# Kernel tuning notes

Measured on AMD Instinct MI355X. Metric: run time of the kernel, lower is better.

## Reference

```python
import jax, jax.numpy as jnp
import numpy as np

C = 1.0          # ball curvature (Manifold default)
EPS = 1e-7
MIN_NORM = 1e-15

def _artanh(x):
    return jnp.arctanh(jnp.clip(x, -1.0 + EPS, 1.0 - EPS))

def _expmap0(u):
    # exp map at origin of the Poincare ball
    n = jnp.clip(jnp.linalg.norm(u, axis=-1, keepdims=True), MIN_NORM, None)
    sc = np.sqrt(C).astype(np.float32)
    return jnp.tanh(sc * n) * u / (sc * n)

def _mobius_add(x, y):
    x2 = jnp.sum(x * x, axis=-1, keepdims=True)
    y2 = jnp.sum(y * y, axis=-1, keepdims=True)
    xy = jnp.sum(x * y, axis=-1, keepdims=True)
    num = (1.0 + 2.0 * C * xy + C * y2) * x + (1.0 - C * x2) * y
    den = 1.0 + 2.0 * C * xy + C * C * x2 * y2
    return num / jnp.clip(den, MIN_NORM, None)

def setup_inputs() -> dict:
    key = jax.random.key(0)
    k1, k2, k3, k4 = jax.random.split(key, 4)
    N, D, U = 8192, 256, 128
    features = jax.random.normal(k1, (N, D), jnp.float32) * 0.1
    adj = jax.random.randint(k2, (N, N), 0, 2, jnp.int32)
    kernel = jax.random.normal(k3, (D, U), jnp.float32) * (1.0 / np.sqrt(D)).astype(np.float32)
    bias = jax.random.normal(k4, (U,), jnp.float32) * 0.01
    return {"features": features, "adj": adj, "kernel": kernel, "bias": bias}

def reference(features, adj, kernel, bias):
    sc = np.sqrt(C).astype(np.float32)
    # dense matmul then lift to the ball
    x = _expmap0(features @ kernel)                     # [N, U]
    # pairwise hyperbolic distance via closed form of ||mobius_add(-x_i, x_j)||
    x2 = jnp.sum(x * x, axis=-1)                        # [N]
    xy = x @ x.T                                        # [N, N]
    A = 1.0 - 2.0 * C * xy + C * x2[None, :]            # [N, N]
    B = (1.0 - C * x2)[:, None]                         # [N, 1]
    num_sq = A * A * x2[:, None] - 2.0 * A * B * xy + B * B * x2[None, :]
    den = 1.0 - 2.0 * C * xy + C * C * x2[:, None] * x2[None, :]
    mnorm = jnp.sqrt(jnp.clip(num_sq, 0.0, None)) / jnp.clip(den, MIN_NORM, None)
    dist = (2.0 / sc) * _artanh(sc * mnorm)             # sqdist ** 0.5 == distance, [N, N]
    # adjacency-masked softmax (zeros -> -inf, as in tf.where(a != 0, a, float.min))
    a = dist * adj.astype(dist.dtype)
    a = jnp.where(a != 0, a, jnp.finfo(a.dtype).min)
    att = jax.nn.softmax(a, axis=-1)                    # [N, N]
    # mobius_matvec with exchange=True: hyperbolic analogue of att @ x (row-wise norm rescale)
    mx = att @ x                                        # [N, U]
    x_n = jnp.clip(jnp.sqrt(x2)[:, None], MIN_NORM, None)
    mx_n = jnp.clip(jnp.linalg.norm(mx, axis=-1, keepdims=True), MIN_NORM, None)
    out = jnp.tanh(mx_n / x_n * _artanh(sc * x_n)) * mx / (sc * mx_n)
    # hyperbolic bias
    b = _expmap0(bias[None, :])                         # [1, U]
    return _mobius_add(out, b)
```

## Files before the change

### kernel.cpp

```cpp
#include <hip/hip_runtime.h>
#include <hip/hip_bf16.h>
#include <math.h>

#define Nn 8192
#define Dd 256
#define Uu 128
#define MI 16
#define NJC 8
#define JCL (Nn / NJC)
#define TJ 32
#define NIT (JCL / TJ)

typedef __attribute__((ext_vector_type(4))) float f32x4;
typedef __attribute__((ext_vector_type(8))) short s16x8;
typedef __attribute__((ext_vector_type(4))) short s16x4;

#define MFMA_K32(a, b, c) __builtin_amdgcn_mfma_f32_16x16x32_bf16((a), (b), (c), 0, 0, 0)

#define GL_LDS(src, dst)                                                              \
  __builtin_amdgcn_global_load_lds(                                                   \
      (const __attribute__((address_space(1))) unsigned int*)(src),                   \
      (__attribute__((address_space(3))) unsigned int*)(dst), 16, 0, 0)

__device__ __forceinline__ f32x4 mfma_k16(s16x4 a, s16x4 b, f32x4 c){
#if __has_builtin(__builtin_amdgcn_mfma_f32_16x16x16bf16_1k)
  return __builtin_amdgcn_mfma_f32_16x16x16bf16_1k(a, b, c, 0, 0, 0);
#else
  asm("v_mfma_f32_16x16x16_bf16 %0, %1, %2, %0" : "+v"(c) : "v"(a), "v"(b));
  return c;
#endif
}

__device__ __forceinline__ short f2bf(float f){
  unsigned int u = __float_as_uint(f);
  u += 0x7fffu + ((u >> 16) & 1u);
  return (short)(u >> 16);
}

__device__ __forceinline__ float waveSum(float v){
  #pragma unroll
  for (int off = 32; off >= 1; off >>= 1) v += __shfl_xor(v, off);
  return v;
}

__global__ __launch_bounds__(256) void k_prep(const float* __restrict__ feat,
                                              const float* __restrict__ kern,
                                              const float* __restrict__ bias,
                                              short* __restrict__ xh,
                                              short* __restrict__ v4,
                                              float* __restrict__ x2,
                                              float* __restrict__ bb){
  const int t = threadIdx.x;
  const int u = t & 127;
  const int g = t >> 7;
  const int n0 = blockIdx.x * 16;
  __shared__ float fS[16][Dd];
  __shared__ float red[4][8];
  __shared__ float redb[4];
  {
    const f32x4* fg = (const f32x4*)(feat + (size_t)n0 * Dd);
    f32x4* fd = (f32x4*)fS;
    #pragma unroll
    for (int c = 0; c < 4; ++c) fd[c * 256 + t] = fg[c * 256 + t];
  }
  __syncthreads();
  float zz[8];
  #pragma unroll
  for (int r = 0; r < 8; ++r) zz[r] = 0.f;
  for (int dq = 0; dq < 64; ++dq){
    const int d = dq * 4;
    const float k0 = kern[(size_t)(d + 0) * Uu + u];
    const float k1 = kern[(size_t)(d + 1) * Uu + u];
    const float k2 = kern[(size_t)(d + 2) * Uu + u];
    const float k3 = kern[(size_t)(d + 3) * Uu + u];
    #pragma unroll
    for (int r = 0; r < 8; ++r){
      const f32x4 f4 = *(const f32x4*)&fS[g * 8 + r][d];
      zz[r] = fmaf(f4.x, k0, fmaf(f4.y, k1, fmaf(f4.z, k2, fmaf(f4.w, k3, zz[r]))));
    }
  }
  #pragma unroll
  for (int r = 0; r < 8; ++r){
    float v = waveSum(zz[r] * zz[r]);
    if ((t & 63) == 0) red[t >> 6][r] = v;
  }
  __syncthreads();
  float scl[8];
  #pragma unroll
  for (int r = 0; r < 8; ++r){
    const float ns  = (g == 0) ? (red[0][r] + red[1][r]) : (red[2][r] + red[3][r]);
    const float nrm = fmaxf(sqrtf(ns), 1e-15f);
    const float th  = tanhf(nrm);
    scl[r] = th / nrm;
    xh[(size_t)(n0 + g * 8 + r) * Uu + u] = f2bf(zz[r] * scl[r]);
  }
  {
    short* vt = v4 + (size_t)blockIdx.x * 2048 + (size_t)(u >> 4) * 256 + (u & 15) * 4;
    #pragma unroll
    for (int qq = 0; qq < 2; ++qq){
      s16x4 w;
      #pragma unroll
      for (int e = 0; e < 4; ++e) w[e] = f2bf(zz[qq * 4 + e] * scl[qq * 4 + e]);
      *(s16x4*)(vt + (g * 2 + qq) * 64) = w;
    }
  }
  if (t < 16){
    const float ns  = (t < 8) ? (red[0][t] + red[1][t]) : (red[2][t - 8] + red[3][t - 8]);
    const float nrm = fmaxf(sqrtf(ns), 1e-15f);
    const float th  = tanhf(nrm);
    x2[n0 + t] = th * th;
  }
  if (blockIdx.x == 0){
    const float bv = (t < 128) ? bias[t] : 0.f;
    float v = waveSum(bv * bv);
    if ((t & 63) == 0) redb[t >> 6] = v;
    __syncthreads();
    const float n2  = redb[0] + redb[1] + redb[2] + redb[3];
    const float nrm = fmaxf(sqrtf(n2), 1e-15f);
    const float th  = tanhf(nrm);
    if (t < 128) bb[t] = bv * th / nrm;
    if (t == 0) bb[Uu] = th * th;
  }
}

__global__ __launch_bounds__(256, 4) void k_attn(const int* __restrict__ adj,
                                                 const short* __restrict__ xh,
                                                 const short* __restrict__ v4,
                                                 const float* __restrict__ x2g,
                                                 float* __restrict__ Opart,
                                                 float* __restrict__ lpart){
  const int t    = threadIdx.x;
  const int lane = t & 63;
  const int wid  = t >> 6;
  const int l15  = lane & 15;
  const int q4   = lane >> 4;
  const int ig   = blockIdx.x >> 3;
  const int jc   = blockIdx.x & 7;
  const int i0   = ig * 64 + wid * 16;
  const int irow = i0 + l15;
  const int jbase = jc * JCL;

  __shared__ __align__(16) short kb[2][4096];
  __shared__ __align__(16) short vb[2][4096];
  __shared__ __align__(16) float x2S[JCL];

  const char* ksrcW = (const char*)xh + (size_t)jbase * 256
                      + l15 * 256 + wid * 64 + q4 * 16;
  const char* vsrcW = (const char*)v4 + (size_t)(jbase >> 4) * 4096
                      + wid * 1024 + lane * 16;

  GL_LDS(ksrcW,        (char*)&kb[0][0] + wid * 1024);
  GL_LDS(ksrcW + 4096, (char*)&kb[0][0] + 4096 + wid * 1024);
  GL_LDS(vsrcW,        (char*)&vb[0][0] + wid * 1024);
  GL_LDS(vsrcW + 4096, (char*)&vb[0][0] + 4096 + wid * 1024);
  GL_LDS((const char*)(x2g + jbase) + wid * 1024 + lane * 16, (char*)x2S + wid * 1024);

  s16x8 qf[4];
  {
    const short* qp = xh + (size_t)irow * Uu + q4 * 8;
    #pragma unroll
    for (int kk = 0; kk < 4; ++kk) qf[kk] = *(const s16x8*)(qp + kk * 32);
  }
  const float x2i  = x2g[irow];
  const float Bv   = 1.f - x2i;
  const float Bv2j = Bv * Bv;
  const float nBv2 = -2.f * Bv;

  f32x4 oc[8];
  #pragma unroll
  for (int uc = 0; uc < 8; ++uc) oc[uc] = (f32x4){0.f, 0.f, 0.f, 0.f};
  float lacc = 0.f;

  const int itDiag = ((i0 >> 10) == jc) ? ((i0 & 1023) >> 5) : -1;
  const int sDiag  = (i0 >> 4) & 1;

  const int* ap = adj + (size_t)irow * Nn + jbase + q4 * 4;

  int4 aqA0 = *(const int4*)(ap);
  int4 aqA1 = *(const int4*)(ap + 16);
  int4 aqB0 = *(const int4*)(ap + 32);
  int4 aqB1 = *(const int4*)(ap + 48);

  asm volatile("s_waitcnt vmcnt(0)" ::: "memory");
  __builtin_amdgcn_s_barrier();
  __builtin_amdgcn_sched_barrier(0);

  #pragma unroll 1
  for (int it = 0; it < NIT; ++it){
    const int cur = it & 1;
    if (it + 1 < NIT){
      const size_t o = (size_t)(it + 1) * 8192;
      GL_LDS(ksrcW + o,        (char*)&kb[cur ^ 1][0] + wid * 1024);
      GL_LDS(ksrcW + o + 4096, (char*)&kb[cur ^ 1][0] + 4096 + wid * 1024);
      GL_LDS(vsrcW + o,        (char*)&vb[cur ^ 1][0] + wid * 1024);
      GL_LDS(vsrcW + o + 4096, (char*)&vb[cur ^ 1][0] + 4096 + wid * 1024);
    }
    __builtin_amdgcn_sched_barrier(0);
    const int itn = (it + 2 < NIT) ? (it + 2) : (NIT - 1);
    const int4 aqN0 = *(const int4*)(ap + itn * 32);
    const int4 aqN1 = *(const int4*)(ap + itn * 32 + 16);
    __builtin_amdgcn_sched_barrier(0);

    #pragma unroll
    for (int sdx = 0; sdx < 2; ++sdx){
      const char* kbp = (const char*)&kb[cur][0] + sdx * 4096;
      const char* vbp = (const char*)&vb[cur][0] + sdx * 4096;
      s16x8 kf[4];
      #pragma unroll
      for (int kk = 0; kk < 4; ++kk)
        kf[kk] = *(const s16x8*)(kbp + kk * 1024 + lane * 16);
      f32x4 s = {0.f, 0.f, 0.f, 0.f};
      s = MFMA_K32(kf[0], qf[0], s);
      s = MFMA_K32(kf[1], qf[1], s);
      s = MFMA_K32(kf[2], qf[2], s);
      s = MFMA_K32(kf[3], qf[3], s);

      const f32x4 x2j = *(const f32x4*)&x2S[it * TJ + sdx * 16 + q4 * 4];
      const int4  aq  = sdx ? aqA1 : aqA0;
      const int aarr[4] = {aq.x, aq.y, aq.z, aq.w};
      float pv[4];
      #pragma unroll
      for (int r = 0; r < 4; ++r){
        const float xy  = s[r];
        const float x2v = x2j[r];
        const float Aa  = fmaf(-2.f, xy, 1.f + x2v);
        const float num = fmaf(Aa * Aa, x2i, fmaf(nBv2 * Aa, xy, Bv2j * x2v));
        const float den = fmaf(x2i, x2v, fmaf(-2.f, xy, 1.f));
        const float sq  = __builtin_amdgcn_sqrtf(fmaxf(num, 0.f));
        const float pd  = fmaxf(den - sq, 1e-30f);
        const float p   = fminf((den + sq) * __builtin_amdgcn_rcpf(pd), 2.0e7f);
        const bool keep = (aarr[r] != 0) && (sq != 0.f);
        pv[r] = keep ? p : 0.f;
      }
      if (it == itDiag && sdx == sDiag){
        const int j0 = jbase + it * TJ + sdx * 16;
        #pragma unroll
        for (int r = 0; r < 4; ++r)
          if ((j0 + 4 * q4 + r) == irow) pv[r] = 0.f;
      }
      lacc += (pv[0] + pv[1]) + (pv[2] + pv[3]);
      s16x4 pb;
      #pragma unroll
      for (int r = 0; r < 4; ++r) pb[r] = f2bf(pv[r]);

      s16x4 vf[8];
      #pragma unroll
      for (int uc = 0; uc < 8; ++uc)
        vf[uc] = *(const s16x4*)(vbp + uc * 512 + lane * 8);
      #pragma unroll
      for (int uc = 0; uc < 8; ++uc) oc[uc] = mfma_k16(vf[uc], pb, oc[uc]);
    }

    aqA0 = aqB0; aqA1 = aqB1; aqB0 = aqN0; aqB1 = aqN1;
    asm volatile("s_waitcnt vmcnt(2)" ::: "memory");
    __builtin_amdgcn_s_barrier();
    __builtin_amdgcn_sched_barrier(0);
  }

  lacc += __shfl_xor(lacc, 16);
  lacc += __shfl_xor(lacc, 32);
  if (lane < 16) lpart[(size_t)jc * Nn + i0 + lane] = lacc;
  float* op = Opart + ((size_t)jc * Nn + irow) * Uu + q4 * 4;
  #pragma unroll
  for (int uc = 0; uc < 8; ++uc) *(f32x4*)(op + uc * 16) = oc[uc];
}

__global__ __launch_bounds__(256) void k_out(const float* __restrict__ Opart,
                                             const float* __restrict__ lpart,
                                             const float* __restrict__ x2g,
                                             const float* __restrict__ bb,
                                             float* __restrict__ out){
  const int t  = threadIdx.x;
  const int i0 = blockIdx.x * MI;
  const int er = t >> 4;
  const int ec = t & 15;
  float l = 0.f;
  #pragma unroll
  for (int c = 0; c < NJC; ++c) l += lpart[(size_t)c * Nn + i0 + er];
  const float linv = 1.f / fmaxf(l, 1e-30f);
  float mx[8]; float s2 = 0.f;
  #pragma unroll
  for (int k = 0; k < 8; ++k){
    float v = 0.f;
    #pragma unroll
    for (int c = 0; c < NJC; ++c)
      v += Opart[((size_t)c * Nn + i0 + er) * Uu + ec + 16 * k];
    v *= linv;
    mx[k] = v; s2 = fmaf(v, v, s2);
  }
  s2 += __shfl_xor(s2, 1); s2 += __shfl_xor(s2, 2);
  s2 += __shfl_xor(s2, 4); s2 += __shfl_xor(s2, 8);
  const float mx_n = fmaxf(sqrtf(s2), 1e-15f);
  const float x2e  = x2g[i0 + er];
  const float x_n  = fmaxf(sqrtf(x2e), 1e-15f);
  const float xcl  = fminf(x_n, 1.f - 1e-7f);
  const float art  = 0.5f * __logf((1.f + xcl) / (1.f - xcl));
  const float th   = tanhf(mx_n / x_n * art);
  const float rmn  = th / mx_n;
  float o[8], bu[8]; float ob = 0.f;
  #pragma unroll
  for (int k = 0; k < 8; ++k){
    bu[k] = bb[ec + 16 * k];
    o[k]  = mx[k] * rmn;
    ob = fmaf(o[k], bu[k], ob);
  }
  ob += __shfl_xor(ob, 1); ob += __shfl_xor(ob, 2);
  ob += __shfl_xor(ob, 4); ob += __shfl_xor(ob, 8);
  const float o2   = th * th;
  const float b2   = bb[Uu];
  const float cnum = 1.f + 2.f * ob + b2;
  const float cden = fmaf(o2, b2, 1.f + 2.f * ob);
  const float rden = 1.f / fmaxf(cden, 1e-15f);
  const float co   = 1.f - o2;
  #pragma unroll
  for (int k = 0; k < 8; ++k)
    out[(size_t)(i0 + er) * Uu + ec + 16 * k] = (cnum * o[k] + co * bu[k]) * rden;
}

extern "C" void kernel_launch(void* const* d_in, const int* in_sizes, int n_in,
                              void* d_out, int out_size, void* d_ws, size_t ws_size,
                              hipStream_t stream){
  (void)in_sizes; (void)n_in; (void)out_size; (void)ws_size;
  const float* feat = (const float*)d_in[0];
  const int*   adj  = (const int*)d_in[1];
  const float* kern = (const float*)d_in[2];
  const float* bias = (const float*)d_in[3];

  float* Opart = (float*)d_ws;
  float* lpart = Opart + (size_t)NJC * Nn * Uu;
  float* x2    = lpart + (size_t)NJC * Nn;
  float* bbw   = x2 + Nn;
  short* xh    = (short*)(bbw + 132);
  short* v4    = xh + (size_t)Nn * Uu;

  k_prep<<<Nn / 16, 256, 0, stream>>>(feat, kern, bias, xh, v4, x2, bbw);
  k_attn<<<(Nn / 64) * NJC, 256, 0, stream>>>(adj, xh, v4, x2, Opart, lpart);
  k_out <<<Nn / MI, 256, 0, stream>>>(Opart, lpart, x2, bbw, (float*)d_out);
}
```

Before: 459.8 us.

## Pack adjacency into 16-row bitmasks before attention kernel

Adds a pre-pass kernel that reads the int32 adjacency matrix once and packs each group of 16 rows into 16-bit masks per column. The attention kernel then reads these compact masks instead of int32 entries and extracts its row's bit. The main loop's adjacency traffic shrinks, though every call still pays a full read of the 256MB adjacency matrix in the extra pack kernel. The workspace grows by the packed buffer.

```diff
diff --git a/kernel.cpp b/kernel.cpp
--- a/kernel.cpp
+++ b/kernel.cpp
@@ -14,6 +14,8 @@
 typedef __attribute__((ext_vector_type(4))) float f32x4;
 typedef __attribute__((ext_vector_type(8))) short s16x8;
 typedef __attribute__((ext_vector_type(4))) short s16x4;
+typedef __attribute__((ext_vector_type(4))) unsigned short u16x4;
+typedef __attribute__((ext_vector_type(8))) unsigned short u16x8;
 
 #define MFMA_K32(a, b, c) __builtin_amdgcn_mfma_f32_16x16x32_bf16((a), (b), (c), 0, 0, 0)
 
@@ -41,6 +43,25 @@
   #pragma unroll
   for (int off = 32; off >= 1; off >>= 1) v += __shfl_xor(v, off);
   return v;
+}
+
+__global__ __launch_bounds__(256) void k_pack(const int* __restrict__ adj,
+                                              unsigned short* __restrict__ adjp){
+  const int it4 = blockIdx.x >> 2;
+  const int jc0 = (blockIdx.x & 3) << 11;
+  const int j0  = jc0 + threadIdx.x * 8;
+  const int* base = adj + (size_t)it4 * 16 * Nn + j0;
+  unsigned short w0=0,w1=0,w2=0,w3=0,w4=0,w5=0,w6=0,w7=0;
+  #pragma unroll 4
+  for (int b = 0; b < 16; ++b){
+    const int4 a0 = *(const int4*)(base + (size_t)b * Nn);
+    const int4 a1 = *(const int4*)(base + (size_t)b * Nn + 4);
+    const unsigned short m = (unsigned short)(1u << b);
+    if (a0.x) w0 |= m;  if (a0.y) w1 |= m;  if (a0.z) w2 |= m;  if (a0.w) w3 |= m;
+    if (a1.x) w4 |= m;  if (a1.y) w5 |= m;  if (a1.z) w6 |= m;  if (a1.w) w7 |= m;
+  }
+  u16x8 w; w[0]=w0; w[1]=w1; w[2]=w2; w[3]=w3; w[4]=w4; w[5]=w5; w[6]=w6; w[7]=w7;
+  *(u16x8*)(adjp + (size_t)it4 * Nn + j0) = w;
 }
 
 __global__ __launch_bounds__(256) void k_prep(const float* __restrict__ feat,
@@ -123,7 +144,7 @@
   }
 }
 
-__global__ __launch_bounds__(256, 4) void k_attn(const int* __restrict__ adj,
+__global__ __launch_bounds__(256, 4) void k_attn(const unsigned short* __restrict__ adjp,
                                                  const short* __restrict__ xh,
                                                  const short* __restrict__ v4,
                                                  const float* __restrict__ x2g,
@@ -174,12 +195,12 @@
   const int itDiag = ((i0 >> 10) == jc) ? ((i0 & 1023) >> 5) : -1;
   const int sDiag  = (i0 >> 4) & 1;
 
-  const int* ap = adj + (size_t)irow * Nn + jbase + q4 * 4;
-
-  int4 aqA0 = *(const int4*)(ap);
-  int4 aqA1 = *(const int4*)(ap + 16);
-  int4 aqB0 = *(const int4*)(ap + 32);
-  int4 aqB1 = *(const int4*)(ap + 48);
+  const unsigned short* app = adjp + (size_t)(i0 >> 4) * Nn + jbase + q4 * 4;
+
+  u16x4 aqA0 = *(const u16x4*)(app);
+  u16x4 aqA1 = *(const u16x4*)(app + 16);
+  u16x4 aqB0 = *(const u16x4*)(app + 32);
+  u16x4 aqB1 = *(const u16x4*)(app + 48);
 
   asm volatile("s_waitcnt vmcnt(0)" ::: "memory");
   __builtin_amdgcn_s_barrier();
@@ -197,8 +218,8 @@
     }
     __builtin_amdgcn_sched_barrier(0);
     const int itn = (it + 2 < NIT) ? (it + 2) : (NIT - 1);
-    const int4 aqN0 = *(const int4*)(ap + itn * 32);
-    const int4 aqN1 = *(const int4*)(ap + itn * 32 + 16);
+    const u16x4 aqN0 = *(const u16x4*)(app + itn * 32);
+    const u16x4 aqN1 = *(const u16x4*)(app + itn * 32 + 16);
     __builtin_amdgcn_sched_barrier(0);
 
     #pragma unroll
@@ -216,8 +237,7 @@
       s = MFMA_K32(kf[3], qf[3], s);
 
       const f32x4 x2j = *(const f32x4*)&x2S[it * TJ + sdx * 16 + q4 * 4];
-      const int4  aq  = sdx ? aqA1 : aqA0;
-      const int aarr[4] = {aq.x, aq.y, aq.z, aq.w};
+      const u16x4 aq  = sdx ? aqA1 : aqA0;
       float pv[4];
       #pragma unroll
       for (int r = 0; r < 4; ++r){
@@ -229,7 +249,7 @@
         const float sq  = __builtin_amdgcn_sqrtf(fmaxf(num, 0.f));
         const float pd  = fmaxf(den - sq, 1e-30f);
         const float p   = fminf((den + sq) * __builtin_amdgcn_rcpf(pd), 2.0e7f);
-        const bool keep = (aarr[r] != 0) && (sq != 0.f);
+        const bool keep = (((aq[r] >> l15) & 1) != 0) && (sq != 0.f);
         pv[r] = keep ? p : 0.f;
       }
       if (it == itDiag && sdx == sDiag){
@@ -332,8 +352,10 @@
   float* bbw   = x2 + Nn;
   short* xh    = (short*)(bbw + 132);
   short* v4    = xh + (size_t)Nn * Uu;
-
+  unsigned short* adjp = (unsigned short*)(v4 + (size_t)Nn * Uu);
+
+  k_pack<<<(Nn / 16) * 4, 256, 0, stream>>>(adj, adjp);
   k_prep<<<Nn / 16, 256, 0, stream>>>(feat, kern, bias, xh, v4, x2, bbw);
-  k_attn<<<(Nn / 64) * NJC, 256, 0, stream>>>(adj, xh, v4, x2, Opart, lpart);
+  k_attn<<<(Nn / 64) * NJC, 256, 0, stream>>>(adjp, xh, v4, x2, Opart, lpart);
   k_out <<<Nn / MI, 256, 0, stream>>>(Opart, lpart, x2, bbw, (float*)d_out);
 }
```

New measurement: 498.4 us. 1.08x slower.

## Process two row groups per wave and split keys into sixteen chunks

Applied to the files above, without the earlier changes.

Each wave now computes attention for 32 query rows instead of 16, reusing each loaded K/V tile for two sets of MFMAs. The key dimension is split into 16 chunks instead of 8 to keep the grid size, with occupancy hint lowered to 2 blocks. This aims to cut LDS and K/V load traffic per useful MFMA, at the cost of more registers, a shorter adjacency prefetch distance, and doubled partial-output traffic for the final reduction.

```diff
diff --git a/kernel.cpp b/kernel.cpp
--- a/kernel.cpp
+++ b/kernel.cpp
@@ -6,7 +6,7 @@
 #define Dd 256
 #define Uu 128
 #define MI 16
-#define NJC 8
+#define NJC 16
 #define JCL (Nn / NJC)
 #define TJ 32
 #define NIT (JCL / TJ)
@@ -123,7 +123,7 @@
   }
 }
 
-__global__ __launch_bounds__(256, 4) void k_attn(const int* __restrict__ adj,
+__global__ __launch_bounds__(256, 2) void k_attn(const int* __restrict__ adj,
                                                  const short* __restrict__ xh,
                                                  const short* __restrict__ v4,
                                                  const float* __restrict__ x2g,
@@ -134,10 +134,9 @@
   const int wid  = t >> 6;
   const int l15  = lane & 15;
   const int q4   = lane >> 4;
-  const int ig   = blockIdx.x >> 3;
-  const int jc   = blockIdx.x & 7;
-  const int i0   = ig * 64 + wid * 16;
-  const int irow = i0 + l15;
+  const int ig   = blockIdx.x >> 4;
+  const int jc   = blockIdx.x & 15;
+  const int i0   = ig * 128 + wid * 32;
   const int jbase = jc * JCL;
 
   __shared__ __align__(16) short kb[2][4096];
@@ -153,33 +152,42 @@
   GL_LDS(ksrcW + 4096, (char*)&kb[0][0] + 4096 + wid * 1024);
   GL_LDS(vsrcW,        (char*)&vb[0][0] + wid * 1024);
   GL_LDS(vsrcW + 4096, (char*)&vb[0][0] + 4096 + wid * 1024);
-  GL_LDS((const char*)(x2g + jbase) + wid * 1024 + lane * 16, (char*)x2S + wid * 1024);
-
-  s16x8 qf[4];
-  {
+  if (wid < 2)
+    GL_LDS((const char*)(x2g + jbase) + wid * 1024 + lane * 16, (char*)x2S + wid * 1024);
+
+  s16x8 qf[2][4];
+  float x2i[2], Bv2j[2], nBv2[2];
+  int   itDiag[2], sDiag[2];
+  #pragma unroll
+  for (int g = 0; g < 2; ++g){
+    const int irow = i0 + g * 16 + l15;
     const short* qp = xh + (size_t)irow * Uu + q4 * 8;
     #pragma unroll
-    for (int kk = 0; kk < 4; ++kk) qf[kk] = *(const s16x8*)(qp + kk * 32);
-  }
-  const float x2i  = x2g[irow];
-  const float Bv   = 1.f - x2i;
-  const float Bv2j = Bv * Bv;
-  const float nBv2 = -2.f * Bv;
-
-  f32x4 oc[8];
-  #pragma unroll
-  for (int uc = 0; uc < 8; ++uc) oc[uc] = (f32x4){0.f, 0.f, 0.f, 0.f};
-  float lacc = 0.f;
-
-  const int itDiag = ((i0 >> 10) == jc) ? ((i0 & 1023) >> 5) : -1;
-  const int sDiag  = (i0 >> 4) & 1;
-
-  const int* ap = adj + (size_t)irow * Nn + jbase + q4 * 4;
-
-  int4 aqA0 = *(const int4*)(ap);
-  int4 aqA1 = *(const int4*)(ap + 16);
-  int4 aqB0 = *(const int4*)(ap + 32);
-  int4 aqB1 = *(const int4*)(ap + 48);
+    for (int kk = 0; kk < 4; ++kk) qf[g][kk] = *(const s16x8*)(qp + kk * 32);
+    const float xi = x2g[irow];
+    x2i[g]  = xi;
+    const float Bv = 1.f - xi;
+    Bv2j[g] = Bv * Bv;
+    nBv2[g] = -2.f * Bv;
+    const int i0g = i0 + g * 16;
+    itDiag[g] = ((i0g >> 9) == jc) ? ((i0g & 511) >> 5) : -1;
+    sDiag[g]  = (i0g >> 4) & 1;
+  }
+
+  f32x4 oc[2][8];
+  #pragma unroll
+  for (int g = 0; g < 2; ++g)
+    #pragma unroll
+    for (int uc = 0; uc < 8; ++uc) oc[g][uc] = (f32x4){0.f, 0.f, 0.f, 0.f};
+  float lacc[2] = {0.f, 0.f};
+
+  const int* ap0 = adj + (size_t)(i0 + l15) * Nn + jbase + q4 * 4;
+  const int* ap1 = adj + (size_t)(i0 + 16 + l15) * Nn + jbase + q4 * 4;
+  int4 aqC[4];
+  aqC[0] = *(const int4*)(ap0);
+  aqC[1] = *(const int4*)(ap0 + 16);
+  aqC[2] = *(const int4*)(ap1);
+  aqC[3] = *(const int4*)(ap1 + 16);
 
   asm volatile("s_waitcnt vmcnt(0)" ::: "memory");
   __builtin_amdgcn_s_barrier();
@@ -196,9 +204,12 @@
       GL_LDS(vsrcW + o + 4096, (char*)&vb[cur ^ 1][0] + 4096 + wid * 1024);
     }
     __builtin_amdgcn_sched_barrier(0);
-    const int itn = (it + 2 < NIT) ? (it + 2) : (NIT - 1);
-    const int4 aqN0 = *(const int4*)(ap + itn * 32);
-    const int4 aqN1 = *(const int4*)(ap + itn * 32 + 16);
+    const int itn = (it + 1 < NIT) ? (it + 1) : (NIT - 1);
+    int4 aqN[4];
+    aqN[0] = *(const int4*)(ap0 + itn * 32);
+    aqN[1] = *(const int4*)(ap0 + itn * 32 + 16);
+    aqN[2] = *(const int4*)(ap1 + itn * 32);
+    aqN[3] = *(const int4*)(ap1 + itn * 32 + 16);
     __builtin_amdgcn_sched_barrier(0);
 
     #pragma unroll
@@ -209,60 +220,76 @@
       #pragma unroll
       for (int kk = 0; kk < 4; ++kk)
         kf[kk] = *(const s16x8*)(kbp + kk * 1024 + lane * 16);
-      f32x4 s = {0.f, 0.f, 0.f, 0.f};
-      s = MFMA_K32(kf[0], qf[0], s);
-      s = MFMA_K32(kf[1], qf[1], s);
-      s = MFMA_K32(kf[2], qf[2], s);
-      s = MFMA_K32(kf[3], qf[3], s);
-
+      f32x4 s0 = {0.f, 0.f, 0.f, 0.f};
+      f32x4 s1 = {0.f, 0.f, 0.f, 0.f};
+      #pragma unroll
+      for (int kk = 0; kk < 4; ++kk){
+        s0 = MFMA_K32(kf[kk], qf[0][kk], s0);
+        s1 = MFMA_K32(kf[kk], qf[1][kk], s1);
+      }
       const f32x4 x2j = *(const f32x4*)&x2S[it * TJ + sdx * 16 + q4 * 4];
-      const int4  aq  = sdx ? aqA1 : aqA0;
-      const int aarr[4] = {aq.x, aq.y, aq.z, aq.w};
-      float pv[4];
-      #pragma unroll
-      for (int r = 0; r < 4; ++r){
-        const float xy  = s[r];
-        const float x2v = x2j[r];
-        const float Aa  = fmaf(-2.f, xy, 1.f + x2v);
-        const float num = fmaf(Aa * Aa, x2i, fmaf(nBv2 * Aa, xy, Bv2j * x2v));
-        const float den = fmaf(x2i, x2v, fmaf(-2.f, xy, 1.f));
-        const float sq  = __builtin_amdgcn_sqrtf(fmaxf(num, 0.f));
-        const float pd  = fmaxf(den - sq, 1e-30f);
-        const float p   = fminf((den + sq) * __builtin_amdgcn_rcpf(pd), 2.0e7f);
-        const bool keep = (aarr[r] != 0) && (sq != 0.f);
-        pv[r] = keep ? p : 0.f;
-      }
-      if (it == itDiag && sdx == sDiag){
-        const int j0 = jbase + it * TJ + sdx * 16;
-        #pragma unroll
-        for (int r = 0; r < 4; ++r)
-          if ((j0 + 4 * q4 + r) == irow) pv[r] = 0.f;
-      }
-      lacc += (pv[0] + pv[1]) + (pv[2] + pv[3]);
-      s16x4 pb;
-      #pragma unroll
-      for (int r = 0; r < 4; ++r) pb[r] = f2bf(pv[r]);
-
       s16x4 vf[8];
       #pragma unroll
       for (int uc = 0; uc < 8; ++uc)
         vf[uc] = *(const s16x4*)(vbp + uc * 512 + lane * 8);
-      #pragma unroll
-      for (int uc = 0; uc < 8; ++uc) oc[uc] = mfma_k16(vf[uc], pb, oc[uc]);
+
+      s16x4 pbg[2];
+      #pragma unroll
+      for (int g = 0; g < 2; ++g){
+        const f32x4 sv = g ? s1 : s0;
+        const int4  aq = aqC[g * 2 + sdx];
+        const int aarr[4] = {aq.x, aq.y, aq.z, aq.w};
+        float pv[4];
+        #pragma unroll
+        for (int r = 0; r < 4; ++r){
+          const float xy  = sv[r];
+          const float x2v = x2j[r];
+          const float Aa  = fmaf(-2.f, xy, 1.f + x2v);
+          const float num = fmaf(Aa * Aa, x2i[g], fmaf(nBv2[g] * Aa, xy, Bv2j[g] * x2v));
+          const float den = fmaf(x2i[g], x2v, fmaf(-2.f, xy, 1.f));
+          const float sq  = __builtin_amdgcn_sqrtf(fmaxf(num, 0.f));
+          const float pd  = fmaxf(den - sq, 1e-30f);
+          const float p   = fminf((den + sq) * __builtin_amdgcn_rcpf(pd), 2.0e7f);
+          const bool keep = (aarr[r] != 0) && (sq != 0.f);
+          pv[r] = keep ? p : 0.f;
+        }
+        if (it == itDiag[g] && sdx == sDiag[g]){
+          const int j0 = jbase + it * TJ + sdx * 16;
+          const int irow = i0 + g * 16 + l15;
+          #pragma unroll
+          for (int r = 0; r < 4; ++r)
+            if ((j0 + 4 * q4 + r) == irow) pv[r] = 0.f;
+        }
+        lacc[g] += (pv[0] + pv[1]) + (pv[2] + pv[3]);
+        s16x4 pb;
+        #pragma unroll
+        for (int r = 0; r < 4; ++r) pb[r] = f2bf(pv[r]);
+        pbg[g] = pb;
+      }
+
+      #pragma unroll
+      for (int uc = 0; uc < 8; ++uc){
+        oc[0][uc] = mfma_k16(vf[uc], pbg[0], oc[0][uc]);
+        oc[1][uc] = mfma_k16(vf[uc], pbg[1], oc[1][uc]);
+      }
     }
 
-    aqA0 = aqB0; aqA1 = aqB1; aqB0 = aqN0; aqB1 = aqN1;
-    asm volatile("s_waitcnt vmcnt(2)" ::: "memory");
+    aqC[0] = aqN[0]; aqC[1] = aqN[1]; aqC[2] = aqN[2]; aqC[3] = aqN[3];
+    asm volatile("s_waitcnt vmcnt(4)" ::: "memory");
     __builtin_amdgcn_s_barrier();
     __builtin_amdgcn_sched_barrier(0);
   }
 
-  lacc += __shfl_xor(lacc, 16);
-  lacc += __shfl_xor(lacc, 32);
-  if (lane < 16) lpart[(size_t)jc * Nn + i0 + lane] = lacc;
-  float* op = Opart + ((size_t)jc * Nn + irow) * Uu + q4 * 4;
-  #pragma unroll
-  for (int uc = 0; uc < 8; ++uc) *(f32x4*)(op + uc * 16) = oc[uc];
+  #pragma unroll
+  for (int g = 0; g < 2; ++g){
+    float la = lacc[g];
+    la += __shfl_xor(la, 16);
+    la += __shfl_xor(la, 32);
+    if (lane < 16) lpart[(size_t)jc * Nn + i0 + g * 16 + lane] = la;
+    float* op = Opart + ((size_t)jc * Nn + i0 + g * 16 + l15) * Uu + q4 * 4;
+    #pragma unroll
+    for (int uc = 0; uc < 8; ++uc) *(f32x4*)(op + uc * 16) = oc[g][uc];
+  }
 }
 
 __global__ __launch_bounds__(256) void k_out(const float* __restrict__ Opart,
@@ -334,6 +361,6 @@
   short* v4    = xh + (size_t)Nn * Uu;
 
   k_prep<<<Nn / 16, 256, 0, stream>>>(feat, kern, bias, xh, v4, x2, bbw);
-  k_attn<<<(Nn / 64) * NJC, 256, 0, stream>>>(adj, xh, v4, x2, Opart, lpart);
+  k_attn<<<(Nn / 128) * NJC, 256, 0, stream>>>(adj, xh, v4, x2, Opart, lpart);
   k_out <<<Nn / MI, 256, 0, stream>>>(Opart, lpart, x2, bbw, (float*)d_out);
 }
```

Result: faster. 445.9 us (-3.0%).
